# Performance work log

Hardware: AMD Instinct MI355X
Metric: run time of the kernel (lower is better)

## Reference

```python
import jax, jax.numpy as jnp
import numpy as np

D_MODEL = 1024
D_INNER = 2048
D_STATE = 16
D_CONV = 4
DT_RANK = 64
RANK = 16
LORA_SCALING = 2.0  # alpha/rank = 32/16
BATCH = 2
SEQLEN = 2048


def setup_inputs() -> dict:
    key = jax.random.key(0)
    ks = jax.random.split(key, 14)
    s = lambda i, shape, sc=1.0: jax.random.normal(ks[i], shape, dtype=jnp.float32) * sc
    return {
        "x": s(0, (BATCH, SEQLEN, D_MODEL)),
        # adapted in_proj (base Linear bias=False + masked LoRA)
        "w_in": s(1, (2 * D_INNER, D_MODEL), 0.02),
        "lora_A_in": s(2, (RANK, D_MODEL), 0.01),
        "lora_B_in": s(3, (2 * D_INNER, RANK), 0.01),
        "mask_in": jnp.ones((2 * D_INNER,), jnp.float32),
        # depthwise causal conv1d
        "conv_w": s(4, (D_INNER, 1, D_CONV), 0.1),
        "conv_b": s(5, (D_INNER,), 0.1),
        # x_proj (bias=False) and dt_proj
        "w_xproj": s(6, (DT_RANK + 2 * D_STATE, D_INNER), 0.02),
        "w_dt": s(7, (D_INNER, DT_RANK), 0.02),
        "b_dt": s(8, (D_INNER,), 0.1),
        # SSM params (S4D-real init for A_log)
        "A_log": jnp.log(jnp.tile(jnp.arange(1, D_STATE + 1, dtype=jnp.float32), (D_INNER, 1))),
        "Dp": s(9, (D_INNER,), 0.1) + 1.0,
        # adapted out_proj
        "w_out": s(10, (D_MODEL, D_INNER), 0.02),
        "lora_A_out": s(11, (RANK, D_INNER), 0.01),
        "lora_B_out": s(12, (D_MODEL, RANK), 0.01),
        "mask_out": jnp.ones((D_MODEL,), jnp.float32),
    }


def _lora_linear(x, w, a, b, mask, scaling):
    # base Linear (bias=False) + sparsity-masked LoRA update
    base = x @ w.T
    lora = ((x @ a.T) @ b.T) * mask * scaling
    return base + lora


def _selective_scan(u, delta, A, Bm, Cm, Dp):
    # u, delta: [B,L,D]; Bm, Cm: [B,L,N]; A: [D,N]; Dp: [D]
    def step(h, inp):
        d_t, b_t, c_t, u_t = inp  # [B,D], [B,N], [B,N], [B,D]
        dA = jnp.exp(d_t[..., None] * A)                     # [B,D,N]
        h = dA * h + (d_t * u_t)[..., None] * b_t[:, None, :]
        y = jnp.sum(h * c_t[:, None, :], axis=-1)            # [B,D]
        return h, y

    Bsz, L, Dd = u.shape
    h0 = jnp.zeros((Bsz, Dd, A.shape[1]), u.dtype)
    xs = (jnp.moveaxis(delta, 1, 0), jnp.moveaxis(Bm, 1, 0),
          jnp.moveaxis(Cm, 1, 0), jnp.moveaxis(u, 1, 0))
    _, ys = jax.lax.scan(step, h0, xs)
    return jnp.moveaxis(ys, 0, 1) + u * Dp


def reference(x, w_in, lora_A_in, lora_B_in, mask_in, conv_w, conv_b,
              w_xproj, w_dt, b_dt, A_log, Dp, w_out, lora_A_out,
              lora_B_out, mask_out):
    B, L, _ = x.shape
    # adapted in_proj -> [B,L,2*d_inner], split into x and gate z
    xz = _lora_linear(x, w_in, lora_A_in, lora_B_in, mask_in, LORA_SCALING)
    xs, z = jnp.split(xz, 2, axis=-1)
    # depthwise causal conv1d (torch pads d_conv-1 both sides then slices [:L])
    xc = jnp.moveaxis(xs, 1, 2)  # [B,D,L]
    xc = jax.lax.conv_general_dilated(
        xc, conv_w, window_strides=(1,), padding=[(D_CONV - 1, 0)],
        feature_group_count=D_INNER,
        dimension_numbers=("NCH", "OIH", "NCH")) + conv_b[None, :, None]
    xs = jax.nn.silu(jnp.moveaxis(xc, 1, 2))  # [B,L,D]
    # input-dependent SSM params
    x_dbl = xs @ w_xproj.T
    dt, Bm, Cm = jnp.split(x_dbl, [DT_RANK, DT_RANK + D_STATE], axis=-1)
    delta = jax.nn.softplus(dt @ w_dt.T + b_dt)  # [B,L,D]
    A = -jnp.exp(A_log)                          # [D,N]
    y = _selective_scan(xs, delta, A, Bm, Cm, Dp)
    y = y * jax.nn.silu(z)
    # adapted out_proj
    return _lora_linear(y, w_out, lora_A_out, lora_B_out, mask_out, LORA_SCALING)
```

## Files before the change

kernel.cpp:

```cpp
#include <hip/hip_runtime.h>
#include <hip/hip_bf16.h>
#include <hip/hip_fp16.h>
#include <cstdint>
#include <cstddef>

#define D_MODEL 1024
#define D_INNER 2048
#define NSTATE  16
#define DTRANK  64
#define BATCH   2
#define SEQLEN  2048
#define BL      (BATCH*SEQLEN)
#define NSEG    64
#define TSEG    (SEQLEN/NSEG)
#define SKX     8
#define KCH     (D_INNER/SKX)
#define LOG2E   1.4426950408889634f
#define HF_BASE ((size_t)NSEG * BATCH * D_INNER * 16)

typedef __attribute__((ext_vector_type(8))) _Float16 f16x8;
typedef __attribute__((ext_vector_type(4))) float f32x4;

__device__ __forceinline__ float softplusf(float x) {
    return fmaxf(x, 0.f) + log1pf(expf(-fabsf(x)));
}
__device__ __forceinline__ unsigned short f2h(float x) {
    __half h = __float2half(x);
    return *(unsigned short*)&h;
}
__device__ __forceinline__ float h2f(unsigned short u) {
    __half h; *(unsigned short*)&h = u;
    return __half2float(h);
}
__device__ __forceinline__ float* hfp(float* xzb, size_t i) {
    return xzb + (i >> 11) * 4096 + (i & 2047);
}
__device__ __forceinline__ const float* hfpc(const float* xzb, size_t i) {
    return xzb + (i >> 11) * 4096 + (i & 2047);
}
__device__ __forceinline__ void gll16(const void* g, void* l) {
    __builtin_amdgcn_global_load_lds(
        (const __attribute__((address_space(1))) void*)g,
        (__attribute__((address_space(3))) void*)l, 16, 0, 0);
}

__global__ __launch_bounds__(256) void premul_kernel(
        const float* __restrict__ lb, const float* __restrict__ mask,
        float* __restrict__ out, int total) {
    int i = blockIdx.x * 256 + threadIdx.x;
    if (i < total) out[i] = lb[i] * mask[i >> 4] * 2.0f;
}

__global__ __launch_bounds__(256) void lora_t_kernel(
        const float* __restrict__ X, int ldx,
        const float* __restrict__ LA, int K,
        float* __restrict__ T) {
    int m = blockIdx.x;
    int r = threadIdx.x >> 4;
    int l = threadIdx.x & 15;
    const float* xrow = X + (size_t)m * ldx;
    const float* arow = LA + (size_t)r * K;
    float s = 0.f;
    for (int k = 4 * l; k < K; k += 64) {
        float4 xv = *(const float4*)(xrow + k);
        float4 av = *(const float4*)(arow + k);
        s += xv.x * av.x + xv.y * av.y + xv.z * av.z + xv.w * av.w;
    }
    #pragma unroll
    for (int o = 8; o; o >>= 1) s += __shfl_xor(s, o, 16);
    if (l == 0) T[(size_t)m * 16 + r] = s;
}

__global__ __launch_bounds__(256) void fused_y16_kernel(
        const float* __restrict__ y, const float* __restrict__ lA,
        unsigned short* __restrict__ A16, int KP, float* __restrict__ T) {
    const int m = blockIdx.x, tid = threadIdx.x;
    const float* yr = y + (size_t)m * 2048;
    float4 v0 = *(const float4*)(yr + tid * 8);
    float4 v1 = *(const float4*)(yr + tid * 8 + 4);
    float yv[8] = {v0.x, v0.y, v0.z, v0.w, v1.x, v1.y, v1.z, v1.w};
    ushort4 h0 = {f2h(yv[0]), f2h(yv[1]), f2h(yv[2]), f2h(yv[3])};
    ushort4 h1 = {f2h(yv[4]), f2h(yv[5]), f2h(yv[6]), f2h(yv[7])};
    *(ushort4*)(A16 + (size_t)m * KP + tid * 8)     = h0;
    *(ushort4*)(A16 + (size_t)m * KP + tid * 8 + 4) = h1;
    float p[16];
    #pragma unroll
    for (int r = 0; r < 16; ++r) {
        const float* lr = lA + (size_t)r * 2048 + tid * 8;
        float4 a0 = *(const float4*)lr;
        float4 a1 = *(const float4*)(lr + 4);
        p[r] = yv[0]*a0.x + yv[1]*a0.y + yv[2]*a0.z + yv[3]*a0.w
             + yv[4]*a1.x + yv[5]*a1.y + yv[6]*a1.z + yv[7]*a1.w;
    }
    #pragma unroll
    for (int r = 0; r < 16; ++r)
        #pragma unroll
        for (int o = 32; o; o >>= 1) p[r] += __shfl_xor(p[r], o);
    __shared__ float red[4][16];
    const int lane = tid & 63, wv = tid >> 6;
    if (lane == 0) {
        #pragma unroll
        for (int r = 0; r < 16; ++r) red[wv][r] = p[r];
    }
    __syncthreads();
    if (tid < 16)
        T[(size_t)m * 16 + tid] = (red[0][tid] + red[1][tid]) + (red[2][tid] + red[3][tid]);
}

__global__ __launch_bounds__(256) void cvt16_kernel(
        const float* __restrict__ src, int lda, int K4, int KP,
        unsigned short* __restrict__ dst, int total4) {
    int idx = blockIdx.x * 256 + threadIdx.x;
    if (idx >= total4) return;
    int m = idx / K4;
    int kq = idx - m * K4;
    float4 v = *(const float4*)(src + (size_t)m * lda + kq * 4);
    ushort4 h;
    h.x = f2h(v.x); h.y = f2h(v.y); h.z = f2h(v.z); h.w = f2h(v.w);
    *(ushort4*)(dst + (size_t)m * KP + kq * 4) = h;
}

__global__ __launch_bounds__(256) void cvtpad16_kernel(
        const float* __restrict__ src, int Msrc, int K4,
        unsigned short* __restrict__ dst, int total4) {
    int idx = blockIdx.x * 256 + threadIdx.x;
    if (idx >= total4) return;
    int m = idx / K4;
    int kq = idx - m * K4;
    ushort4 h = {0, 0, 0, 0};
    if (m < Msrc) {
        float4 v = *(const float4*)(src + (size_t)m * (K4 * 4) + kq * 4);
        h.x = f2h(v.x); h.y = f2h(v.y); h.z = f2h(v.z); h.w = f2h(v.w);
    }
    *(ushort4*)(dst + (size_t)m * (K4 * 4) + kq * 4) = h;
}

__global__ __launch_bounds__(256) void ext16_kernel(
        const float* __restrict__ t16, int K, int KP, int ncols,
        unsigned short* __restrict__ dst, int M) {
    int idx = blockIdx.x * 256 + threadIdx.x;
    if (idx >= M * ncols) return;
    int c = idx % ncols, m = idx / ncols;
    unsigned short hv = 0;
    if (c < 16) hv = f2h(t16[(size_t)m * 16 + c]);
    dst[(size_t)m * KP + K + c] = hv;
}

template<int EPI>
__global__ __launch_bounds__(256, 4) void mfma_gemm16(
        const unsigned short* __restrict__ Ag, const unsigned short* __restrict__ Wg,
        int KP, float* __restrict__ C, int ldc,
        const float* __restrict__ bias, int Nbound, int kchunk) {
    __shared__ __align__(16) short Ash[2][4][128][8];
    __shared__ __align__(16) short Wsh[2][4][128][8];
    const int tid = threadIdx.x;
    const int bn0 = blockIdx.x * 128, bm0 = blockIdx.y * 128;
    const int wave = tid >> 6, lane = tid & 63;
    const int wr = (wave >> 1) * 64, wc = (wave & 1) * 64;
    const int fr = lane & 15, fg = lane >> 4;
    int koff0 = 0, KT;
    if (kchunk) {
        koff0 = blockIdx.z * kchunk;
        KT = kchunk >> 5;
        C += (size_t)blockIdx.z * gridDim.y * 128 * ldc;
    } else {
        KT = KP >> 5;
    }
    const int srow = tid & 127, skg = tid >> 7;

    const unsigned short* pA = Ag + (size_t)(bm0 + srow) * KP + koff0 + skg * 8;
    const unsigned short* pW = Wg + (size_t)(bn0 + srow) * KP + koff0 + skg * 8;

    f32x4 acc[4][4];
    #pragma unroll
    for (int i = 0; i < 4; ++i)
        #pragma unroll
        for (int j = 0; j < 4; ++j) acc[i][j] = (f32x4){0.f, 0.f, 0.f, 0.f};

    auto stage = [&](int kt, int pb) {
        const int koff = kt * 32;
        gll16(pA + koff,      &Ash[pb][skg    ][srow][0]);
        gll16(pA + koff + 16, &Ash[pb][skg + 2][srow][0]);
        gll16(pW + koff,      &Wsh[pb][skg    ][srow][0]);
        gll16(pW + koff + 16, &Wsh[pb][skg + 2][srow][0]);
    };

    stage(0, 0);
    for (int kt = 0; kt < KT; ++kt) {
        const int cur = kt & 1;
        __syncthreads();
        if (kt + 1 < KT) stage(kt + 1, cur ^ 1);
        f16x8 a[4], w[4];
        #pragma unroll
        for (int i = 0; i < 4; ++i) {
            a[i] = *(const f16x8*)&Ash[cur][fg][wr + i * 16 + fr][0];
            w[i] = *(const f16x8*)&Wsh[cur][fg][wc + i * 16 + fr][0];
        }
        #pragma unroll
        for (int i = 0; i < 4; ++i)
            #pragma unroll
            for (int j = 0; j < 4; ++j)
                acc[i][j] = __builtin_amdgcn_mfma_f32_16x16x32_f16(a[i], w[j], acc[i][j], 0, 0, 0);
    }
    #pragma unroll
    for (int i = 0; i < 4; ++i) {
        #pragma unroll
        for (int j = 0; j < 4; ++j) {
            int n = bn0 + wc + j * 16 + fr;
            if (n < Nbound) {
                #pragma unroll
                for (int q = 0; q < 4; ++q) {
                    int m = bm0 + wr + i * 16 + fg * 4 + q;
                    float v = acc[i][j][q];
                    if (EPI == 2) v = softplusf(v + bias[n]);
                    C[(size_t)m * ldc + n] = v;
                }
            }
        }
    }
}

__global__ __launch_bounds__(256) void sk2_reduce_kernel(
        const float* __restrict__ p, float* __restrict__ out, int total) {
    int i = blockIdx.x * 256 + threadIdx.x;
    if (i < total) out[i] = p[i] + p[(size_t)total + i];
}

__global__ __launch_bounds__(256) void sk_reduce_kernel(
        const float* __restrict__ part, float* __restrict__ out, int total) {
    int i = blockIdx.x * 256 + threadIdx.x;
    if (i >= total) return;
    float s = 0.f;
    #pragma unroll
    for (int sk = 0; sk < SKX; ++sk) s += part[(size_t)sk * total + i];
    out[i] = s;
}

__global__ __launch_bounds__(256) void conv_silu_kernel(
        const float* __restrict__ xz, const float* __restrict__ cw,
        const float* __restrict__ cb, unsigned short* __restrict__ u16) {
    int idx = blockIdx.x * 256 + threadIdx.x;
    int d  = idx & (D_INNER - 1);
    int bl = idx >> 11;
    int l  = bl & (SEQLEN - 1);
    const float* base = xz + (size_t)bl * 4096 + d;
    float4 w = *(const float4*)(cw + d * 4);
    float s = cb[d];
    if (l >= 3) s = fmaf(base[-3 * 4096], w.x, s);
    if (l >= 2) s = fmaf(base[-2 * 4096], w.y, s);
    if (l >= 1) s = fmaf(base[-1 * 4096], w.z, s);
    s = fmaf(base[0], w.w, s);
    float r = s * __builtin_amdgcn_rcpf(1.f + __expf(-s));
    u16[idx] = f2h(r);
}

__global__ __launch_bounds__(256) void scan_partA(
        const float* __restrict__ delta, const unsigned short* __restrict__ u16,
        const float* __restrict__ xdbl, const float* __restrict__ A_log,
        float* __restrict__ xzws) {
    __shared__ float Bs[TSEG][16];
    const int tid = threadIdx.x;
    const int bx  = blockIdx.x;
    const int seg = bx >> 4;
    const int b   = (bx >> 3) & 1;
    const int d   = (bx & 7) * 256 + tid;
    const int t0  = seg * TSEG;
    {
        const float* bc0 = xdbl + ((size_t)b * SEQLEN + t0) * 96 + 64;
        for (int i = tid; i < TSEG * 16; i += 256)
            Bs[i >> 4][i & 15] = bc0[(size_t)(i >> 4) * 96 + (i & 15)];
    }
    float An2[16];
    #pragma unroll
    for (int q = 0; q < 4; ++q) {
        float4 a = *(const float4*)(A_log + d * 16 + q * 4);
        An2[q*4+0] = -__expf(a.x) * LOG2E;
        An2[q*4+1] = -__expf(a.y) * LOG2E;
        An2[q*4+2] = -__expf(a.z) * LOG2E;
        An2[q*4+3] = -__expf(a.w) * LOG2E;
    }
    const float* dl = delta + ((size_t)b * SEQLEN + t0) * D_INNER + d;
    const unsigned short* uu = u16 + ((size_t)b * SEQLEN + t0) * D_INNER + d;
    float h[16];
    #pragma unroll
    for (int n = 0; n < 16; ++n) h[n] = 0.f;
    float sd = 0.f;
    float pdv[4], puv[4];
    #pragma unroll
    for (int j = 0; j < 4; ++j) {
        pdv[j] = dl[(size_t)j * D_INNER];
        puv[j] = h2f(uu[(size_t)j * D_INNER]);
    }
    __syncthreads();
    for (int t4 = 0; t4 < TSEG; t4 += 4) {
        #pragma unroll
        for (int j = 0; j < 4; ++j) {
            const float dv = pdv[j], uv = puv[j];
            if (t4 + 4 < TSEG) {
                pdv[j] = dl[(size_t)(t4 + 4 + j) * D_INNER];
                puv[j] = h2f(uu[(size_t)(t4 + 4 + j) * D_INNER]);
            }
            const float dvuv = dv * uv;
            sd += dv;
            #pragma unroll
            for (int n = 0; n < 16; ++n)
                h[n] = fmaf(exp2f(dv * An2[n]), h[n], dvuv * Bs[t4 + j][n]);
        }
    }
    const size_t o = (size_t)seg * (BATCH * D_INNER) + (size_t)b * D_INNER + d;
    #pragma unroll
    for (int q = 0; q < 4; ++q)
        *(float4*)hfp(xzws, o * 16 + q * 4) =
            make_float4(h[q*4], h[q*4+1], h[q*4+2], h[q*4+3]);
    *hfp(xzws, HF_BASE + o) = sd;
}

__global__ __launch_bounds__(256) void scan_combine(
        const float* __restrict__ A_log, float* xzws) {
    int idx = blockIdx.x * 256 + threadIdx.x;
    int n = idx & 15, row = idx >> 4;
    int d = row & (D_INNER - 1);
    float An = -__expf(A_log[d * 16 + n]);
    float h = 0.f;
    float f[4], sdv[4];
    #pragma unroll
    for (int j = 0; j < 4; ++j) {
        size_t o = (size_t)j * (BATCH * D_INNER) + row;
        f[j]   = *hfpc(xzws, o * 16 + n);
        sdv[j] = *hfpc(xzws, HF_BASE + o);
    }
    for (int s4 = 0; s4 < NSEG; s4 += 4) {
        float nf[4], nsd[4];
        if (s4 + 4 < NSEG) {
            #pragma unroll
            for (int j = 0; j < 4; ++j) {
                size_t o = (size_t)(s4 + 4 + j) * (BATCH * D_INNER) + row;
                nf[j]  = *hfpc(xzws, o * 16 + n);
                nsd[j] = *hfpc(xzws, HF_BASE + o);
            }
        }
        #pragma unroll
        for (int j = 0; j < 4; ++j) {
            size_t o = (size_t)(s4 + j) * (BATCH * D_INNER) + row;
            *hfp(xzws, o * 16 + n) = h;
            h = fmaf(__expf(An * sdv[j]), h, f[j]);
        }
        #pragma unroll
        for (int j = 0; j < 4; ++j) { f[j] = nf[j]; sdv[j] = nsd[j]; }
    }
}

__global__ __launch_bounds__(256) void scan_partB(
        const float* delta, const unsigned short* __restrict__ u16,
        const float* __restrict__ xdbl, const float* __restrict__ xz,
        const float* __restrict__ A_log, const float* __restrict__ Dp,
        float* yg) {
    __shared__ float BCs[TSEG][32];
    const int tid = threadIdx.x;
    const int bx  = blockIdx.x;
    const int seg = bx >> 4;
    const int b   = (bx >> 3) & 1;
    const int d   = (bx & 7) * 256 + tid;
    const int t0  = seg * TSEG;
    {
        const float* bc0 = xdbl + ((size_t)b * SEQLEN + t0) * 96 + 64;
        for (int i = tid; i < TSEG * 32; i += 256)
            BCs[i >> 5][i & 31] = bc0[(size_t)(i >> 5) * 96 + (i & 31)];
    }
    float An2[16];
    #pragma unroll
    for (int q = 0; q < 4; ++q) {
        float4 a = *(const float4*)(A_log + d * 16 + q * 4);
        An2[q*4+0] = -__expf(a.x) * LOG2E;
        An2[q*4+1] = -__expf(a.y) * LOG2E;
        An2[q*4+2] = -__expf(a.z) * LOG2E;
        An2[q*4+3] = -__expf(a.w) * LOG2E;
    }
    const float Dd = Dp[d];
    const float* dl = delta + ((size_t)b * SEQLEN + t0) * D_INNER + d;
    const unsigned short* uu = u16 + ((size_t)b * SEQLEN + t0) * D_INNER + d;
    const float* zz = xz    + ((size_t)b * SEQLEN + t0) * 4096 + D_INNER + d;
    float* yo = yg + ((size_t)b * SEQLEN + t0) * D_INNER + d;
    const size_t o = (size_t)seg * (BATCH * D_INNER) + (size_t)b * D_INNER + d;
    float h[16];
    #pragma unroll
    for (int q = 0; q < 4; ++q) {
        float4 hv = *(const float4*)hfpc(xz, o * 16 + q * 4);
        h[q*4] = hv.x; h[q*4+1] = hv.y; h[q*4+2] = hv.z; h[q*4+3] = hv.w;
    }
    float pdv[4], puv[4], pzv[4];
    #pragma unroll
    for (int j = 0; j < 4; ++j) {
        pdv[j] = dl[(size_t)j * D_INNER];
        puv[j] = h2f(uu[(size_t)j * D_INNER]);
        pzv[j] = zz[(size_t)j * 4096];
    }
    __syncthreads();
    for (int t4 = 0; t4 < TSEG; t4 += 4) {
        #pragma unroll
        for (int j = 0; j < 4; ++j) {
            const float dv = pdv[j], uv = puv[j], zv = pzv[j];
            if (t4 + 4 < TSEG) {
                pdv[j] = dl[(size_t)(t4 + 4 + j) * D_INNER];
                puv[j] = h2f(uu[(size_t)(t4 + 4 + j) * D_INNER]);
                pzv[j] = zz[(size_t)(t4 + 4 + j) * 4096];
            }
            const float dvuv = dv * uv;
            #pragma unroll
            for (int n = 0; n < 16; ++n)
                h[n] = fmaf(exp2f(dv * An2[n]), h[n], dvuv * BCs[t4 + j][n]);
            float acc[4] = {0.f, 0.f, 0.f, 0.f};
            #pragma unroll
            for (int n = 0; n < 16; ++n)
                acc[n & 3] = fmaf(h[n], BCs[t4 + j][16 + n], acc[n & 3]);
            float yv = fmaf(uv, Dd, (acc[0] + acc[1]) + (acc[2] + acc[3]));
            float sig = zv * __builtin_amdgcn_rcpf(1.f + __expf(-zv));
            yo[(size_t)(t4 + j) * D_INNER] = yv * sig;
        }
    }
}

extern "C" void kernel_launch(void* const* d_in, const int* in_sizes, int n_in,
                              void* d_out, int out_size, void* d_ws, size_t ws_size,
                              hipStream_t stream) {
    const float* x        = (const float*)d_in[0];
    const float* w_in     = (const float*)d_in[1];
    const float* lA_in    = (const float*)d_in[2];
    const float* lB_in    = (const float*)d_in[3];
    const float* mask_in  = (const float*)d_in[4];
    const float* conv_w   = (const float*)d_in[5];
    const float* conv_b   = (const float*)d_in[6];
    const float* w_xp     = (const float*)d_in[7];
    const float* w_dt     = (const float*)d_in[8];
    const float* b_dt     = (const float*)d_in[9];
    const float* A_log    = (const float*)d_in[10];
    const float* Dp       = (const float*)d_in[11];
    const float* w_out    = (const float*)d_in[12];
    const float* lA_out   = (const float*)d_in[13];
    const float* lB_out   = (const float*)d_in[14];
    const float* mask_out = (const float*)d_in[15];

    float* ws    = (float*)d_ws;
    float* xz    = ws;
    float* u     = xz    + (size_t)BL * 4096;
    float* delta = u     + (size_t)BL * D_INNER;
    float* xdbl  = delta + (size_t)BL * D_INNER;
    float* t16   = xdbl  + (size_t)BL * 96;
    float* lbin  = t16   + (size_t)BL * 16;
    float* lbout = lbin  + (size_t)4096 * 16;

    const int KP_IN = 1056;
    unsigned short* A16_in = (unsigned short*)u;
    unsigned short* W16_in = A16_in + (size_t)4096 * KP_IN;
    unsigned short* u16 = (unsigned short*)u;

    const int KP_OUT = 2112, KH_OUT = 1056;
    unsigned short* A16_out = (unsigned short*)xz;
    unsigned short* W16_out = A16_out + (size_t)4096 * KP_OUT;

    float* outf    = (float*)d_out;
    float* xp_part = outf;
    unsigned short* W16_xp = (unsigned short*)(outf + (size_t)SKX * BL * 96);
    unsigned short* A16_dt = (unsigned short*)d_out;
    unsigned short* W16_dt = A16_dt + (size_t)4096 * 64;

    premul_kernel<<<(4096 * 16 + 255) / 256, 256, 0, stream>>>(lB_in, mask_in, lbin, 4096 * 16);
    premul_kernel<<<(1024 * 16 + 255) / 256, 256, 0, stream>>>(lB_out, mask_out, lbout, 1024 * 16);
    lora_t_kernel<<<BL, 256, 0, stream>>>(x, D_MODEL, lA_in, D_MODEL, t16);
    cvt16_kernel<<<4096, 256, 0, stream>>>(x,    1024, 256, KP_IN, A16_in, 4096 * 256);
    cvt16_kernel<<<4096, 256, 0, stream>>>(w_in, 1024, 256, KP_IN, W16_in, 4096 * 256);
    ext16_kernel<<<512, 256, 0, stream>>>(t16,  1024, KP_IN, 32, A16_in, 4096);
    ext16_kernel<<<512, 256, 0, stream>>>(lbin, 1024, KP_IN, 32, W16_in, 4096);
    mfma_gemm16<0><<<dim3(32, 32), 256, 0, stream>>>(
        A16_in, W16_in, KP_IN, xz, 4096, nullptr, 4096, 0);
    conv_silu_kernel<<<(BL * D_INNER) / 256, 256, 0, stream>>>(xz, conv_w, conv_b, u16);
    cvtpad16_kernel<<<(128 * 512 + 255) / 256, 256, 0, stream>>>(w_xp, 96, 512, W16_xp, 128 * 512);
    mfma_gemm16<0><<<dim3(1, 32, SKX), 256, 0, stream>>>(
        u16, W16_xp, 2048, xp_part, 96, nullptr, 96, KCH);
    sk_reduce_kernel<<<(BL * 96 + 255) / 256, 256, 0, stream>>>(xp_part, xdbl, BL * 96);
    cvt16_kernel<<<(4096 * 16 + 255) / 256, 256, 0, stream>>>(xdbl, 96, 16, 64, A16_dt, 4096 * 16);
    cvt16_kernel<<<(2048 * 16 + 255) / 256, 256, 0, stream>>>(w_dt, 64, 16, 64, W16_dt, 2048 * 16);
    mfma_gemm16<2><<<dim3(16, 32), 256, 0, stream>>>(
        A16_dt, W16_dt, 64, delta, 2048, b_dt, 2048, 0);
    scan_partA<<<NSEG * BATCH * 8, 256, 0, stream>>>(delta, u16, xdbl, A_log, xz);
    scan_combine<<<(BATCH * D_INNER * 16) / 256, 256, 0, stream>>>(A_log, xz);
    scan_partB<<<NSEG * BATCH * 8, 256, 0, stream>>>(delta, u16, xdbl, xz, A_log, Dp, delta);
    fused_y16_kernel<<<BL, 256, 0, stream>>>(delta, lA_out, A16_out, KP_OUT, t16);
    cvt16_kernel<<<2048, 256, 0, stream>>>(w_out, 2048, 512, KP_OUT, W16_out, 1024 * 512);
    ext16_kernel<<<(4096 * 64 + 255) / 256, 256, 0, stream>>>(t16,   2048, KP_OUT, 64, A16_out, 4096);
    ext16_kernel<<<(1024 * 64 + 255) / 256, 256, 0, stream>>>(lbout, 2048, KP_OUT, 64, W16_out, 1024);
    float* P = delta;
    mfma_gemm16<0><<<dim3(8, 32, 2), 256, 0, stream>>>(
        A16_out, W16_out, KP_OUT, P, 1024, nullptr, 1024, KH_OUT);
    sk2_reduce_kernel<<<(4096 * 1024) / 256, 256, 0, stream>>>(P, (float*)d_out, 4096 * 1024);
}
```

Measured before the change: 397.5 us.

## Store in_proj output as fp16, split-K out_proj four ways, deepen x_proj split

The in_proj GEMM now writes xz in fp16 through a new epilogue, and conv and scan_partB read the half-precision values. This halves the traffic of the largest intermediate. The scan carry state moves to its own workspace region, which the smaller xz makes room for. The out_proj GEMM is split four ways along K, using padding up to 2176 and partials in two buffers, and x_proj split-K goes from 8 to 16 to give more parallelism. In exchange the gate and conv inputs carry fp16 precision loss, and the extra split-K partials add reduction traffic.

After: 416.5 us. 4.8% more time.

```diff
diff --git a/kernel.cpp b/kernel.cpp
--- a/kernel.cpp
+++ b/kernel.cpp
@@ -13,10 +13,9 @@
 #define BL      (BATCH*SEQLEN)
 #define NSEG    64
 #define TSEG    (SEQLEN/NSEG)
-#define SKX     8
+#define SKX     16
 #define KCH     (D_INNER/SKX)
 #define LOG2E   1.4426950408889634f
-#define HF_BASE ((size_t)NSEG * BATCH * D_INNER * 16)
 
 typedef __attribute__((ext_vector_type(8))) _Float16 f16x8;
 typedef __attribute__((ext_vector_type(4))) float f32x4;
@@ -31,12 +30,6 @@
 __device__ __forceinline__ float h2f(unsigned short u) {
     __half h; *(unsigned short*)&h = u;
     return __half2float(h);
-}
-__device__ __forceinline__ float* hfp(float* xzb, size_t i) {
-    return xzb + (i >> 11) * 4096 + (i & 2047);
-}
-__device__ __forceinline__ const float* hfpc(const float* xzb, size_t i) {
-    return xzb + (i >> 11) * 4096 + (i & 2047);
 }
 __device__ __forceinline__ void gll16(const void* g, void* l) {
     __builtin_amdgcn_global_load_lds(
@@ -150,7 +143,8 @@
 __global__ __launch_bounds__(256, 4) void mfma_gemm16(
         const unsigned short* __restrict__ Ag, const unsigned short* __restrict__ Wg,
         int KP, float* __restrict__ C, int ldc,
-        const float* __restrict__ bias, int Nbound, int kchunk) {
+        const float* __restrict__ bias, int Nbound, int kchunk,
+        float* __restrict__ Calt) {
     __shared__ __align__(16) short Ash[2][4][128][8];
     __shared__ __align__(16) short Wsh[2][4][128][8];
     const int tid = threadIdx.x;
@@ -160,9 +154,15 @@
     const int fr = lane & 15, fg = lane >> 4;
     int koff0 = 0, KT;
     if (kchunk) {
-        koff0 = blockIdx.z * kchunk;
+        int z = blockIdx.z;
+        koff0 = z * kchunk;
         KT = kchunk >> 5;
-        C += (size_t)blockIdx.z * gridDim.y * 128 * ldc;
+        if (Calt) {
+            if (z >= 2) { C = Calt; z -= 2; }
+            C += (size_t)z * gridDim.y * 128 * ldc;
+        } else {
+            C += (size_t)z * gridDim.y * 128 * ldc;
+        }
     } else {
         KT = KP >> 5;
     }
@@ -212,18 +212,24 @@
                 for (int q = 0; q < 4; ++q) {
                     int m = bm0 + wr + i * 16 + fg * 4 + q;
                     float v = acc[i][j][q];
-                    if (EPI == 2) v = softplusf(v + bias[n]);
-                    C[(size_t)m * ldc + n] = v;
+                    if (EPI == 1) {
+                        ((unsigned short*)C)[(size_t)m * ldc + n] = f2h(v);
+                    } else {
+                        if (EPI == 2) v = softplusf(v + bias[n]);
+                        C[(size_t)m * ldc + n] = v;
+                    }
                 }
             }
         }
     }
 }
 
-__global__ __launch_bounds__(256) void sk2_reduce_kernel(
-        const float* __restrict__ p, float* __restrict__ out, int total) {
+__global__ __launch_bounds__(256) void sk4_reduce_kernel(
+        const float* __restrict__ p01, const float* __restrict__ p23,
+        float* __restrict__ out, int total) {
     int i = blockIdx.x * 256 + threadIdx.x;
-    if (i < total) out[i] = p[i] + p[(size_t)total + i];
+    if (i < total)
+        out[i] = (p01[i] + p01[(size_t)total + i]) + (p23[i] + p23[(size_t)total + i]);
 }
 
 __global__ __launch_bounds__(256) void sk_reduce_kernel(
@@ -237,19 +243,19 @@
 }
 
 __global__ __launch_bounds__(256) void conv_silu_kernel(
-        const float* __restrict__ xz, const float* __restrict__ cw,
+        const unsigned short* __restrict__ xz16, const float* __restrict__ cw,
         const float* __restrict__ cb, unsigned short* __restrict__ u16) {
     int idx = blockIdx.x * 256 + threadIdx.x;
     int d  = idx & (D_INNER - 1);
     int bl = idx >> 11;
     int l  = bl & (SEQLEN - 1);
-    const float* base = xz + (size_t)bl * 4096 + d;
+    const unsigned short* base = xz16 + (size_t)bl * 4096 + d;
     float4 w = *(const float4*)(cw + d * 4);
     float s = cb[d];
-    if (l >= 3) s = fmaf(base[-3 * 4096], w.x, s);
-    if (l >= 2) s = fmaf(base[-2 * 4096], w.y, s);
-    if (l >= 1) s = fmaf(base[-1 * 4096], w.z, s);
-    s = fmaf(base[0], w.w, s);
+    if (l >= 3) s = fmaf(h2f(base[-3 * 4096]), w.x, s);
+    if (l >= 2) s = fmaf(h2f(base[-2 * 4096]), w.y, s);
+    if (l >= 1) s = fmaf(h2f(base[-1 * 4096]), w.z, s);
+    s = fmaf(h2f(base[0]), w.w, s);
     float r = s * __builtin_amdgcn_rcpf(1.f + __expf(-s));
     u16[idx] = f2h(r);
 }
@@ -257,7 +263,7 @@
 __global__ __launch_bounds__(256) void scan_partA(
         const float* __restrict__ delta, const unsigned short* __restrict__ u16,
         const float* __restrict__ xdbl, const float* __restrict__ A_log,
-        float* __restrict__ xzws) {
+        float* __restrict__ hF, float* __restrict__ sumd) {
     __shared__ float Bs[TSEG][16];
     const int tid = threadIdx.x;
     const int bx  = blockIdx.x;
@@ -310,13 +316,13 @@
     const size_t o = (size_t)seg * (BATCH * D_INNER) + (size_t)b * D_INNER + d;
     #pragma unroll
     for (int q = 0; q < 4; ++q)
-        *(float4*)hfp(xzws, o * 16 + q * 4) =
+        *(float4*)(hF + o * 16 + q * 4) =
             make_float4(h[q*4], h[q*4+1], h[q*4+2], h[q*4+3]);
-    *hfp(xzws, HF_BASE + o) = sd;
+    sumd[o] = sd;
 }
 
 __global__ __launch_bounds__(256) void scan_combine(
-        const float* __restrict__ A_log, float* xzws) {
+        const float* __restrict__ A_log, float* hF, const float* __restrict__ sumd) {
     int idx = blockIdx.x * 256 + threadIdx.x;
     int n = idx & 15, row = idx >> 4;
     int d = row & (D_INNER - 1);
@@ -326,8 +332,8 @@
     #pragma unroll
     for (int j = 0; j < 4; ++j) {
         size_t o = (size_t)j * (BATCH * D_INNER) + row;
-        f[j]   = *hfpc(xzws, o * 16 + n);
-        sdv[j] = *hfpc(xzws, HF_BASE + o);
+        f[j]   = hF[o * 16 + n];
+        sdv[j] = sumd[o];
     }
     for (int s4 = 0; s4 < NSEG; s4 += 4) {
         float nf[4], nsd[4];
@@ -335,14 +341,14 @@
             #pragma unroll
             for (int j = 0; j < 4; ++j) {
                 size_t o = (size_t)(s4 + 4 + j) * (BATCH * D_INNER) + row;
-                nf[j]  = *hfpc(xzws, o * 16 + n);
-                nsd[j] = *hfpc(xzws, HF_BASE + o);
+                nf[j]  = hF[o * 16 + n];
+                nsd[j] = sumd[o];
             }
         }
         #pragma unroll
         for (int j = 0; j < 4; ++j) {
             size_t o = (size_t)(s4 + j) * (BATCH * D_INNER) + row;
-            *hfp(xzws, o * 16 + n) = h;
+            hF[o * 16 + n] = h;
             h = fmaf(__expf(An * sdv[j]), h, f[j]);
         }
         #pragma unroll
@@ -352,9 +358,9 @@
 
 __global__ __launch_bounds__(256) void scan_partB(
         const float* delta, const unsigned short* __restrict__ u16,
-        const float* __restrict__ xdbl, const float* __restrict__ xz,
+        const float* __restrict__ xdbl, const unsigned short* __restrict__ xz16,
         const float* __restrict__ A_log, const float* __restrict__ Dp,
-        float* yg) {
+        const float* __restrict__ hin, float* yg) {
     __shared__ float BCs[TSEG][32];
     const int tid = threadIdx.x;
     const int bx  = blockIdx.x;
@@ -379,13 +385,13 @@
     const float Dd = Dp[d];
     const float* dl = delta + ((size_t)b * SEQLEN + t0) * D_INNER + d;
     const unsigned short* uu = u16 + ((size_t)b * SEQLEN + t0) * D_INNER + d;
-    const float* zz = xz    + ((size_t)b * SEQLEN + t0) * 4096 + D_INNER + d;
+    const unsigned short* zz = xz16 + ((size_t)b * SEQLEN + t0) * 4096 + D_INNER + d;
     float* yo = yg + ((size_t)b * SEQLEN + t0) * D_INNER + d;
     const size_t o = (size_t)seg * (BATCH * D_INNER) + (size_t)b * D_INNER + d;
     float h[16];
     #pragma unroll
     for (int q = 0; q < 4; ++q) {
-        float4 hv = *(const float4*)hfpc(xz, o * 16 + q * 4);
+        float4 hv = *(const float4*)(hin + o * 16 + q * 4);
         h[q*4] = hv.x; h[q*4+1] = hv.y; h[q*4+2] = hv.z; h[q*4+3] = hv.w;
     }
     float pdv[4], puv[4], pzv[4];
@@ -393,7 +399,7 @@
     for (int j = 0; j < 4; ++j) {
         pdv[j] = dl[(size_t)j * D_INNER];
         puv[j] = h2f(uu[(size_t)j * D_INNER]);
-        pzv[j] = zz[(size_t)j * 4096];
+        pzv[j] = h2f(zz[(size_t)j * 4096]);
     }
     __syncthreads();
     for (int t4 = 0; t4 < TSEG; t4 += 4) {
@@ -403,7 +409,7 @@
             if (t4 + 4 < TSEG) {
                 pdv[j] = dl[(size_t)(t4 + 4 + j) * D_INNER];
                 puv[j] = h2f(uu[(size_t)(t4 + 4 + j) * D_INNER]);
-                pzv[j] = zz[(size_t)(t4 + 4 + j) * 4096];
+                pzv[j] = h2f(zz[(size_t)(t4 + 4 + j) * 4096]);
             }
             const float dvuv = dv * uv;
             #pragma unroll
@@ -449,20 +455,26 @@
     float* lbin  = t16   + (size_t)BL * 16;
     float* lbout = lbin  + (size_t)4096 * 16;
 
+    unsigned short* xz16 = (unsigned short*)xz;
+    float* hF   = xz + (size_t)BL * 2048;
+    float* sumd = hF + (size_t)NSEG * BATCH * D_INNER * 16;
+
     const int KP_IN = 1056;
     unsigned short* A16_in = (unsigned short*)u;
     unsigned short* W16_in = A16_in + (size_t)4096 * KP_IN;
     unsigned short* u16 = (unsigned short*)u;
 
-    const int KP_OUT = 2112, KH_OUT = 1056;
+    const int KP_OUT = 2176, KH_OUT = 544;
     unsigned short* A16_out = (unsigned short*)xz;
     unsigned short* W16_out = A16_out + (size_t)4096 * KP_OUT;
 
-    float* outf    = (float*)d_out;
-    float* xp_part = outf;
-    unsigned short* W16_xp = (unsigned short*)(outf + (size_t)SKX * BL * 96);
-    unsigned short* A16_dt = (unsigned short*)d_out;
+    unsigned short* W16_xp = (unsigned short*)d_out;
+    unsigned short* A16_dt = W16_xp + (size_t)128 * 2048;
     unsigned short* W16_dt = A16_dt + (size_t)4096 * 64;
+
+    float* xp_part = delta;
+    float* P01 = delta;
+    float* P23 = u;
 
     premul_kernel<<<(4096 * 16 + 255) / 256, 256, 0, stream>>>(lB_in, mask_in, lbin, 4096 * 16);
     premul_kernel<<<(1024 * 16 + 255) / 256, 256, 0, stream>>>(lB_out, mask_out, lbout, 1024 * 16);
@@ -471,26 +483,25 @@
     cvt16_kernel<<<4096, 256, 0, stream>>>(w_in, 1024, 256, KP_IN, W16_in, 4096 * 256);
     ext16_kernel<<<512, 256, 0, stream>>>(t16,  1024, KP_IN, 32, A16_in, 4096);
     ext16_kernel<<<512, 256, 0, stream>>>(lbin, 1024, KP_IN, 32, W16_in, 4096);
-    mfma_gemm16<0><<<dim3(32, 32), 256, 0, stream>>>(
-        A16_in, W16_in, KP_IN, xz, 4096, nullptr, 4096, 0);
-    conv_silu_kernel<<<(BL * D_INNER) / 256, 256, 0, stream>>>(xz, conv_w, conv_b, u16);
+    mfma_gemm16<1><<<dim3(32, 32), 256, 0, stream>>>(
+        A16_in, W16_in, KP_IN, (float*)xz16, 4096, nullptr, 4096, 0, nullptr);
+    conv_silu_kernel<<<(BL * D_INNER) / 256, 256, 0, stream>>>(xz16, conv_w, conv_b, u16);
     cvtpad16_kernel<<<(128 * 512 + 255) / 256, 256, 0, stream>>>(w_xp, 96, 512, W16_xp, 128 * 512);
     mfma_gemm16<0><<<dim3(1, 32, SKX), 256, 0, stream>>>(
-        u16, W16_xp, 2048, xp_part, 96, nullptr, 96, KCH);
+        u16, W16_xp, 2048, xp_part, 96, nullptr, 96, KCH, nullptr);
     sk_reduce_kernel<<<(BL * 96 + 255) / 256, 256, 0, stream>>>(xp_part, xdbl, BL * 96);
     cvt16_kernel<<<(4096 * 16 + 255) / 256, 256, 0, stream>>>(xdbl, 96, 16, 64, A16_dt, 4096 * 16);
     cvt16_kernel<<<(2048 * 16 + 255) / 256, 256, 0, stream>>>(w_dt, 64, 16, 64, W16_dt, 2048 * 16);
     mfma_gemm16<2><<<dim3(16, 32), 256, 0, stream>>>(
-        A16_dt, W16_dt, 64, delta, 2048, b_dt, 2048, 0);
-    scan_partA<<<NSEG * BATCH * 8, 256, 0, stream>>>(delta, u16, xdbl, A_log, xz);
-    scan_combine<<<(BATCH * D_INNER * 16) / 256, 256, 0, stream>>>(A_log, xz);
-    scan_partB<<<NSEG * BATCH * 8, 256, 0, stream>>>(delta, u16, xdbl, xz, A_log, Dp, delta);
+        A16_dt, W16_dt, 64, delta, 2048, b_dt, 2048, 0, nullptr);
+    scan_partA<<<NSEG * BATCH * 8, 256, 0, stream>>>(delta, u16, xdbl, A_log, hF, sumd);
+    scan_combine<<<(BATCH * D_INNER * 16) / 256, 256, 0, stream>>>(A_log, hF, sumd);
+    scan_partB<<<NSEG * BATCH * 8, 256, 0, stream>>>(delta, u16, xdbl, xz16, A_log, Dp, hF, delta);
     fused_y16_kernel<<<BL, 256, 0, stream>>>(delta, lA_out, A16_out, KP_OUT, t16);
     cvt16_kernel<<<2048, 256, 0, stream>>>(w_out, 2048, 512, KP_OUT, W16_out, 1024 * 512);
-    ext16_kernel<<<(4096 * 64 + 255) / 256, 256, 0, stream>>>(t16,   2048, KP_OUT, 64, A16_out, 4096);
-    ext16_kernel<<<(1024 * 64 + 255) / 256, 256, 0, stream>>>(lbout, 2048, KP_OUT, 64, W16_out, 1024);
-    float* P = delta;
-    mfma_gemm16<0><<<dim3(8, 32, 2), 256, 0, stream>>>(
-        A16_out, W16_out, KP_OUT, P, 1024, nullptr, 1024, KH_OUT);
-    sk2_reduce_kernel<<<(4096 * 1024) / 256, 256, 0, stream>>>(P, (float*)d_out, 4096 * 1024);
-}
+    ext16_kernel<<<(4096 * 128 + 255) / 256, 256, 0, stream>>>(t16,   2048, KP_OUT, 128, A16_out, 4096);
+    ext16_kernel<<<(1024 * 128 + 255) / 256, 256, 0, stream>>>(lbout, 2048, KP_OUT, 128, W16_out, 1024);
+    mfma_gemm16<0><<<dim3(8, 32, 4), 256, 0, stream>>>(
+        A16_out, W16_out, KP_OUT, P01, 1024, nullptr, 1024, KH_OUT, P23);
+    sk4_reduce_kernel<<<(4096 * 1024) / 256, 256, 0, stream>>>(P01, P23, (float*)d_out, 4096 * 1024);
+}
```
